# Optimization experiments

Hardware: AMD Instinct MI355X
Metric: run time of the kernel (lower is better)

## Reference

```python
import jax, jax.numpy as jnp
import numpy as np
from jax import lax

B, C, W, H = 32, 64, 32, 32
HEADS, RED = 4, 16
D = C // HEADS


def setup_inputs() -> dict:
    key = jax.random.key(0)
    ks = jax.random.split(key, 16)
    s = 0.05
    return {
        "x": jax.random.normal(ks[0], (B, C, W, H), jnp.float32),
        "Wq": jax.random.normal(ks[1], (C, C), jnp.float32) * s,
        "bq": jnp.zeros((C,), jnp.float32),
        "Wk": jax.random.normal(ks[2], (C, C), jnp.float32) * s,
        "bk": jnp.zeros((C,), jnp.float32),
        "Wv": jax.random.normal(ks[3], (C, C), jnp.float32) * s,
        "bv": jnp.zeros((C,), jnp.float32),
        "rel_h": jax.random.normal(ks[4], (1, HEADS, D, 1, H), jnp.float32),
        "rel_w": jax.random.normal(ks[5], (1, HEADS, D, W, 1), jnp.float32),
        "ln_g": jnp.ones((C, W, H), jnp.float32),
        "ln_b": jnp.zeros((C, W, H), jnp.float32),
        "ca_w1": jax.random.normal(ks[6], (C // RED, C), jnp.float32) * s,
        "ca_b1": jnp.zeros((C // RED,), jnp.float32),
        "ca_w2": jax.random.normal(ks[7], (C, C // RED), jnp.float32) * s,
        "ca_b2": jnp.zeros((C,), jnp.float32),
        "sa_w": jax.random.normal(ks[8], (1, 2, 7, 7), jnp.float32) * s,
        "sa_b": jnp.zeros((1,), jnp.float32),
    }


def reference(x, Wq, bq, Wk, bk, Wv, bv, rel_h, rel_w, ln_g, ln_b,
              ca_w1, ca_b1, ca_w2, ca_b2, sa_w, sa_b):
    b, c, w, h = x.shape
    n = w * h
    d = c // HEADS

    def conv1x1(t, wt, bt):
        return jnp.einsum('bchw,oc->bohw', t, wt) + bt[None, :, None, None]

    # ---- MHSA branch ----
    q = conv1x1(x, Wq, bq).reshape(b, HEADS, d, n)
    k = conv1x1(x, Wk, bk).reshape(b, HEADS, d, n)
    v = conv1x1(x, Wv, bv).reshape(b, HEADS, d, n)
    cc = jnp.einsum('bhdi,bhdj->bhij', q, k)                  # content-content
    pos = (rel_h + rel_w).reshape(1, HEADS, d, n)              # [1,H,d,N]
    cp = jnp.einsum('zhdi,bhdj->bhij', pos, q)                 # content-position
    att = jax.nn.softmax(cc + cp, axis=-1)                     # [b,H,N,N]
    out = jnp.einsum('bhdj,bhij->bhdi', v, att).reshape(b, c, w, h)
    # LayerNorm over (C,W,H)
    mu = jnp.mean(out, axis=(1, 2, 3), keepdims=True)
    var = jnp.var(out, axis=(1, 2, 3), keepdims=True)
    ln = (out - mu) * lax.rsqrt(var + 1e-5) * ln_g[None] + ln_b[None]
    mhsa = ln + x

    # ---- CBAM branch ----
    avg = jnp.mean(x, axis=(2, 3))                             # [b,c]
    mx = jnp.max(x, axis=(2, 3))

    def mlp(f):
        hid = jax.nn.relu(jnp.einsum('bc,oc->bo', f, ca_w1) + ca_b1)
        return jnp.einsum('bc,oc->bo', hid, ca_w2) + ca_b2

    ch_att = jax.nn.sigmoid(mlp(avg) + mlp(mx))[:, :, None, None]
    xc = ch_att * x
    feat = jnp.stack([jnp.mean(xc, axis=1), jnp.max(xc, axis=1)], axis=1)  # [b,2,w,h]
    sp = lax.conv_general_dilated(feat, sa_w, (1, 1), 'SAME',
                                  dimension_numbers=('NCHW', 'OIHW', 'NCHW'))
    sp = sp + sa_b[None, :, None, None]
    cbam = jax.nn.sigmoid(sp) * xc

    return mhsa + cbam + x
```

## Files before the change

kernel.cpp:

```cpp
#include <hip/hip_runtime.h>
#include <hip/hip_bf16.h>

#define BB 32
#define CC 64
#define WW 32
#define HHT 32
#define NH 4
#define DHD 16
#define NN 1024
#define LOG2E 1.4426950408889634f

typedef __attribute__((ext_vector_type(8))) short bf16x8;
typedef __attribute__((ext_vector_type(4))) float f32x4;

__device__ __forceinline__ float wave_sum(float v) {
#pragma unroll
  for (int off = 32; off > 0; off >>= 1) v += __shfl_down(v, off, 64);
  return v;
}
__device__ __forceinline__ float wave_max(float v) {
#pragma unroll
  for (int off = 32; off > 0; off >>= 1) v = fmaxf(v, __shfl_down(v, off, 64));
  return v;
}
__device__ __forceinline__ unsigned packbf2(float lo, float hi) {
  union { __hip_bfloat162 h; unsigned u; } c;
  c.h = __float22bfloat162_rn(float2{lo, hi});
  return c.u;
}
__device__ __forceinline__ short bf16s(float f) {
  unsigned a = __float_as_uint(f);
  a += 0x7FFFu + ((a >> 16) & 1u);
  return (short)(a >> 16);
}

__global__ __launch_bounds__(256) void qkv_kernel(
    const float* __restrict__ x,
    const float* __restrict__ Wq, const float* __restrict__ bq,
    const float* __restrict__ Wk, const float* __restrict__ bk,
    const float* __restrict__ Wv, const float* __restrict__ bv,
    short* __restrict__ KQ, short* __restrict__ Vb, float* __restrict__ lnzero)
{
  __shared__ __align__(16) short Ws[192 * 72];
  const int tid = threadIdx.x;
  const int b = blockIdx.y, nt = blockIdx.x;

  if (tid < 192) {
    const int m = tid >> 4, dd = tid & 15;
    const int mat = m >> 2, h = m & 3;
    const float* src = (mat == 0 ? Wk : (mat == 1 ? Wq : Wv)) + (h * 16 + dd) * CC;
    const float scale = (mat == 0) ? LOG2E : 1.f;
    short* dst = Ws + tid * 72;
#pragma unroll
    for (int c8 = 0; c8 < 8; ++c8) {
      const float4 f0 = *reinterpret_cast<const float4*>(src + c8 * 8);
      const float4 f1 = *reinterpret_cast<const float4*>(src + c8 * 8 + 4);
      uint4 u;
      u.x = packbf2(f0.x*scale, f0.y*scale); u.y = packbf2(f0.z*scale, f0.w*scale);
      u.z = packbf2(f1.x*scale, f1.y*scale); u.w = packbf2(f1.z*scale, f1.w*scale);
      *reinterpret_cast<uint4*>(dst + c8 * 8) = u;
    }
  }
  if (blockIdx.x == 0 && blockIdx.y == 0 && tid < 64) lnzero[tid] = 0.f;
  __syncthreads();

  const int wid = tid >> 6, lane = tid & 63, Q = lane >> 4, il = lane & 15;
  const int n = nt * 64 + wid * 16 + il;
  const float* xb = x + (size_t)b * CC * NN;

  union { bf16x8 s; unsigned u[4]; } bfr[2];
#pragma unroll
  for (int half = 0; half < 2; ++half) {
#pragma unroll
    for (int p = 0; p < 4; ++p) {
      const int c0 = 32 * half + 8 * Q + 2 * p;
      const float f0 = xb[(size_t)c0 * NN + n];
      const float f1 = xb[(size_t)(c0 + 1) * NN + n];
      bfr[half].u[p] = packbf2(f0, f1);
    }
  }

  const f32x4 zero4 = {0.f, 0.f, 0.f, 0.f};
  f32x4 acc[12];
#pragma unroll
  for (int m = 0; m < 12; ++m) {
    const short* wr = Ws + (m * 16 + il) * 72;
    const bf16x8 a0 = *reinterpret_cast<const bf16x8*>(wr + 8 * Q);
    const bf16x8 a1 = *reinterpret_cast<const bf16x8*>(wr + 32 + 8 * Q);
    acc[m] = __builtin_amdgcn_mfma_f32_16x16x32_bf16(a0, bfr[0].s, zero4, 0, 0, 0);
    acc[m] = __builtin_amdgcn_mfma_f32_16x16x32_bf16(a1, bfr[1].s, acc[m], 0, 0, 0);
  }

#pragma unroll
  for (int m = 0; m < 12; ++m) {
    const int mat = m >> 2, h = m & 3;
    const float bsc = (mat == 0) ? LOG2E : 1.f;
    const float4 bias = *reinterpret_cast<const float4*>(
        (mat == 0 ? bk : (mat == 1 ? bq : bv)) + h * 16 + 4 * Q);
    const float v0 = acc[m][0] + bias.x*bsc, v1 = acc[m][1] + bias.y*bsc;
    const float v2 = acc[m][2] + bias.z*bsc, v3 = acc[m][3] + bias.w*bsc;
    if (mat < 2) {
      uint2 pk;
      pk.x = packbf2(v0, v1); pk.y = packbf2(v2, v3);
      *reinterpret_cast<uint2*>(KQ + ((size_t)(b * NH + h) * NN + n) * 32 +
                                (mat == 0 ? 0 : 16) + 4 * Q) = pk;
    } else {
      short* vb = Vb + ((size_t)(b * NH + h) * 16 + 4 * Q) * NN + n;
      vb[0]            = bf16s(v0);
      vb[(size_t)NN]   = bf16s(v1);
      vb[2*(size_t)NN] = bf16s(v2);
      vb[3*(size_t)NN] = bf16s(v3);
    }
  }
}

__global__ __launch_bounds__(256, 3) void flash_kernel(
    const short* __restrict__ KQ, const short* __restrict__ Vb,
    const float* __restrict__ rel_h, const float* __restrict__ rel_w,
    float* __restrict__ attnout, float* __restrict__ lnsum, float* __restrict__ lnsum2)
{
  const int tid = threadIdx.x;
  const int wid = tid >> 6, lane = tid & 63;
  const int Q = lane >> 4, il = lane & 15;
  const int bh = blockIdx.x;
  const int h = bh & 3, b = bh >> 2;
  const int pr = wid & 1;
  const int jh = wid >> 1;
  const int ibase = blockIdx.y * 128 + pr * 64;
  const int j0base = jh * 512;

  bf16x8 bfrag[4];
#pragma unroll
  for (int g2 = 0; g2 < 4; ++g2) {
    const int i = ibase + g2*16 + il;
    if (Q < 2) {
      bfrag[g2] = *reinterpret_cast<const bf16x8*>(KQ + ((size_t)bh*NN + i)*32 + 16 + 8*Q);
    } else {
      const int wrow = i >> 5, hcol = i & 31;
      union { bf16x8 s; unsigned u[4]; } t;
#pragma unroll
      for (int p = 0; p < 4; ++p) {
        const int d0 = 8*(Q-2) + 2*p;
        const float f0 = LOG2E*(rel_h[(h*DHD + d0)*HHT + hcol] + rel_w[(h*DHD + d0)*WW + wrow]);
        const float f1 = LOG2E*(rel_h[(h*DHD + d0+1)*HHT + hcol] + rel_w[(h*DHD + d0+1)*WW + wrow]);
        t.u[p] = packbf2(f0, f1);
      }
      bfrag[g2] = t.s;
    }
  }

  const short* KQb = KQ + (size_t)bh*NN*32;
  const short* Vbb = Vb + ((size_t)bh*16 + il)*NN;
  const f32x4 zero4 = {0.f, 0.f, 0.f, 0.f};
  f32x4 acc[4]  = {zero4, zero4, zero4, zero4};
  f32x4 lacc[4] = {zero4, zero4, zero4, zero4};
  union u32x4 { bf16x8 s; unsigned u[4]; };
  u32x4 ones;
  ones.u[0] = ones.u[1] = ones.u[2] = ones.u[3] = 0x3F803F80u;

  bf16x8 agc[4], agn[4];
  u32x4 bv0c, bv1c, bv0n, bv1n;

#define LOADTILE(T, AG, BV0, BV1)                                              \
  {                                                                            \
    const int j0_ = j0base + ((T) & 7) * 64;                                   \
    _Pragma("unroll")                                                          \
    for (int g_ = 0; g_ < 4; ++g_)                                             \
      AG[g_] = *reinterpret_cast<const bf16x8*>(                               \
          KQb + (size_t)(j0_ + 16*g_ + il)*32 + 8*Q);                          \
    const short* vp_ = Vbb + j0_ + 4*Q;                                        \
    const uint2 l0_ = *reinterpret_cast<const uint2*>(vp_);                    \
    const uint2 h0_ = *reinterpret_cast<const uint2*>(vp_ + 16);               \
    const uint2 l1_ = *reinterpret_cast<const uint2*>(vp_ + 32);               \
    const uint2 h1_ = *reinterpret_cast<const uint2*>(vp_ + 48);               \
    BV0.u[0] = l0_.x; BV0.u[1] = l0_.y; BV0.u[2] = h0_.x; BV0.u[3] = h0_.y;    \
    BV1.u[0] = l1_.x; BV1.u[1] = l1_.y; BV1.u[2] = h1_.x; BV1.u[3] = h1_.y;    \
  }

#define FINISH(GP, B0, B1)                                                     \
  {                                                                            \
    unsigned pk_[4][2];                                                        \
    _Pragma("unroll")                                                          \
    for (int g_ = 0; g_ < 4; ++g_) {                                           \
      const float p0_ = __builtin_amdgcn_exp2f(sp[g_][0]);                     \
      const float p1_ = __builtin_amdgcn_exp2f(sp[g_][1]);                     \
      const float p2_ = __builtin_amdgcn_exp2f(sp[g_][2]);                     \
      const float p3_ = __builtin_amdgcn_exp2f(sp[g_][3]);                     \
      pk_[g_][0] = packbf2(p0_, p1_);                                          \
      pk_[g_][1] = packbf2(p2_, p3_);                                          \
    }                                                                          \
    u32x4 ap0_, ap1_;                                                          \
    ap0_.u[0] = pk_[0][0]; ap0_.u[1] = pk_[0][1];                              \
    ap0_.u[2] = pk_[1][0]; ap0_.u[3] = pk_[1][1];                              \
    ap1_.u[0] = pk_[2][0]; ap1_.u[1] = pk_[2][1];                              \
    ap1_.u[2] = pk_[3][0]; ap1_.u[3] = pk_[3][1];                              \
    acc[GP]  = __builtin_amdgcn_mfma_f32_16x16x32_bf16(ap0_.s, B0.s,  acc[GP], 0, 0, 0);  \
    lacc[GP] = __builtin_amdgcn_mfma_f32_16x16x32_bf16(ap0_.s, ones.s, lacc[GP], 0, 0, 0);\
    acc[GP]  = __builtin_amdgcn_mfma_f32_16x16x32_bf16(ap1_.s, B1.s,  acc[GP], 0, 0, 0);  \
    lacc[GP] = __builtin_amdgcn_mfma_f32_16x16x32_bf16(ap1_.s, ones.s, lacc[GP], 0, 0, 0);\
  }

  LOADTILE(0, agc, bv0c, bv1c);
  LOADTILE(1, agn, bv0n, bv1n);
  f32x4 sp[4];
#pragma unroll
  for (int g = 0; g < 4; ++g)
    sp[g] = __builtin_amdgcn_mfma_f32_16x16x32_bf16(agc[g], bfrag[0], zero4, 0, 0, 0);

  for (int t = 0; t < 8; ++t) {
#pragma unroll
    for (int g2 = 1; g2 < 4; ++g2) {
      f32x4 sn[4];
#pragma unroll
      for (int g = 0; g < 4; ++g)
        sn[g] = __builtin_amdgcn_mfma_f32_16x16x32_bf16(agc[g], bfrag[g2], zero4, 0, 0, 0);
      FINISH(g2 - 1, bv0c, bv1c);
#pragma unroll
      for (int g = 0; g < 4; ++g) sp[g] = sn[g];
    }
    if (t < 7) {
      u32x4 b0o = bv0c, b1o = bv1c;
#pragma unroll
      for (int g = 0; g < 4; ++g) agc[g] = agn[g];
      bv0c = bv0n; bv1c = bv1n;
      f32x4 sn[4];
#pragma unroll
      for (int g = 0; g < 4; ++g)
        sn[g] = __builtin_amdgcn_mfma_f32_16x16x32_bf16(agc[g], bfrag[0], zero4, 0, 0, 0);
      FINISH(3, b0o, b1o);
#pragma unroll
      for (int g = 0; g < 4; ++g) sp[g] = sn[g];
      LOADTILE(t + 2, agn, bv0n, bv1n);
    } else {
      FINISH(3, bv0c, bv1c);
    }
  }
#undef LOADTILE
#undef FINISH

  __shared__ float cmb[2][32][64];
  __shared__ float r1[2], r2[2];
  if (jh == 1) {
#pragma unroll
    for (int g2 = 0; g2 < 4; ++g2)
#pragma unroll
      for (int r = 0; r < 4; ++r) {
        cmb[pr][g2*4 + r][lane]      = acc[g2][r];
        cmb[pr][16 + g2*4 + r][lane] = lacc[g2][r];
      }
  }
  __syncthreads();
  if (jh == 0) {
    float s1 = 0.f, s2 = 0.f;
#pragma unroll
    for (int g2 = 0; g2 < 4; ++g2) {
      float4 vv;
      float* vp = &vv.x;
#pragma unroll
      for (int r = 0; r < 4; ++r) {
        const float num = acc[g2][r]  + cmb[pr][g2*4 + r][lane];
        const float den = lacc[g2][r] + cmb[pr][16 + g2*4 + r][lane];
        const float v = num / den;
        vp[r] = v;
        s1 += v; s2 += v*v;
      }
      *reinterpret_cast<float4*>(
          &attnout[((size_t)b*CC + h*DHD + il)*NN + ibase + g2*16 + 4*Q]) = vv;
    }
    s1 = wave_sum(s1); s2 = wave_sum(s2);
    if (lane == 0) { r1[pr] = s1; r2[pr] = s2; }
  }
  __syncthreads();
  if (tid == 0) {
    atomicAdd(&lnsum[b],  r1[0] + r1[1]);
    atomicAdd(&lnsum2[b], r2[0] + r2[1]);
  }
}

__global__ __launch_bounds__(256) void cbamstats_kernel(
    const float* __restrict__ x, float* __restrict__ avg, float* __restrict__ mx)
{
  const int bc = blockIdx.x, tid = threadIdx.x;
  const float* p = x + (size_t)bc*NN;
  float s = 0.f, m = -3.0e38f;
  for (int u = tid; u < NN; u += 256) { const float v = p[u]; s += v; m = fmaxf(m, v); }
  s = wave_sum(s); m = wave_max(m);
  __shared__ float rs[4], rm[4];
  const int wid = tid >> 6, lane = tid & 63;
  if (lane == 0) { rs[wid] = s; rm[wid] = m; }
  __syncthreads();
  if (tid == 0) {
    avg[bc] = (rs[0]+rs[1]+rs[2]+rs[3]) * (1.f/NN);
    mx[bc]  = fmaxf(fmaxf(rm[0], rm[1]), fmaxf(rm[2], rm[3]));
  }
}

__global__ __launch_bounds__(256) void mlpfeat_kernel(
    const float* __restrict__ x, const float* __restrict__ avg, const float* __restrict__ mxv,
    const float* __restrict__ w1, const float* __restrict__ b1,
    const float* __restrict__ w2, const float* __restrict__ b2,
    float* __restrict__ chv, float* __restrict__ feat)
{
  const int b = blockIdx.y, qq = blockIdx.x, tid = threadIdx.x;
  __shared__ float sa[CC], sm[CC], sch[CC];
  __shared__ float ps[4][64], pm[4][64];
  if (tid < CC) { sa[tid] = avg[b*CC + tid]; sm[tid] = mxv[b*CC + tid]; }
  __syncthreads();
  if (tid < CC) {
    float s = 2.f * b2[tid];
#pragma unroll
    for (int o = 0; o < 4; ++o) {
      float ha = b1[o], hm = b1[o];
#pragma unroll
      for (int k = 0; k < CC; ++k) { ha += w1[o*CC + k]*sa[k]; hm += w1[o*CC + k]*sm[k]; }
      s += w2[tid*4 + o] * (fmaxf(ha, 0.f) + fmaxf(hm, 0.f));
    }
    const float c = 1.f/(1.f + __expf(-s));
    sch[tid] = c;
    if (qq == 0) chv[b*CC + tid] = c;
  }
  __syncthreads();
  const int nl = tid & 63, cg = tid >> 6;
  const int n = qq*64 + nl;
  float s = 0.f, m = -3.0e38f;
#pragma unroll
  for (int c = cg*16; c < cg*16 + 16; ++c) {
    const float v = sch[c] * x[((size_t)b*CC + c)*NN + n];
    s += v; m = fmaxf(m, v);
  }
  ps[cg][nl] = s; pm[cg][nl] = m;
  __syncthreads();
  if (cg == 0) {
    const float S = ps[0][nl]+ps[1][nl]+ps[2][nl]+ps[3][nl];
    const float M = fmaxf(fmaxf(pm[0][nl], pm[1][nl]), fmaxf(pm[2][nl], pm[3][nl]));
    feat[(size_t)b*2*NN + n]      = S * (1.f/CC);
    feat[(size_t)b*2*NN + NN + n] = M;
  }
}

__global__ __launch_bounds__(256) void final_kernel(
    const float* __restrict__ x, const float* __restrict__ attn,
    const float* __restrict__ ln_g, const float* __restrict__ ln_b,
    const float* __restrict__ feat, const float* __restrict__ ch,
    const float* __restrict__ lnsum, const float* __restrict__ lnsum2,
    const float* __restrict__ sa_w, const float* __restrict__ sa_b,
    float* __restrict__ out)
{
  const int b = blockIdx.y;
  const int c0 = blockIdx.z * 16;
  const int n = blockIdx.x*256 + threadIdx.x;
  const int w = n >> 5, hh = n & 31;
  __shared__ float sch[CC];
  __shared__ float swt[98];
  if (threadIdx.x < CC) sch[threadIdx.x] = ch[b*CC + threadIdx.x];
  if (threadIdx.x < 98) swt[threadIdx.x] = sa_w[threadIdx.x];
  __syncthreads();

  float s = sa_b[0];
#pragma unroll
  for (int ci = 0; ci < 2; ++ci)
#pragma unroll
    for (int kh = 0; kh < 7; ++kh) {
      const int wy = w + kh - 3;
      if (wy < 0 || wy >= WW) continue;
#pragma unroll
      for (int kw = 0; kw < 7; ++kw) {
        const int hx = hh + kw - 3;
        if (hx < 0 || hx >= HHT) continue;
        s += feat[((size_t)(b*2) + ci)*NN + wy*HHT + hx] * swt[ci*49 + kh*7 + kw];
      }
    }
  const float sg = 1.f/(1.f + __expf(-s));
  const float inv = 1.f/(CC*NN);
  const float m = lnsum[b]*inv;
  const float var = lnsum2[b]*inv - m*m;
  const float r = rsqrtf(var + 1e-5f);
#pragma unroll
  for (int c = c0; c < c0 + 16; ++c) {
    const size_t idx = ((size_t)b*CC + c)*NN + n;
    const float xa = x[idx];
    const float ln = (attn[idx] - m) * r * ln_g[c*NN + n] + ln_b[c*NN + n];
    out[idx] = ln + 2.f*xa + sg * sch[c] * xa;
  }
}

extern "C" void kernel_launch(void* const* d_in, const int* in_sizes, int n_in,
                              void* d_out, int out_size, void* d_ws, size_t ws_size,
                              hipStream_t stream)
{
  const float* x     = (const float*)d_in[0];
  const float* Wq    = (const float*)d_in[1];
  const float* bq    = (const float*)d_in[2];
  const float* Wk    = (const float*)d_in[3];
  const float* bk    = (const float*)d_in[4];
  const float* Wv    = (const float*)d_in[5];
  const float* bv    = (const float*)d_in[6];
  const float* rel_h = (const float*)d_in[7];
  const float* rel_w = (const float*)d_in[8];
  const float* ln_g  = (const float*)d_in[9];
  const float* ln_b  = (const float*)d_in[10];
  const float* cw1   = (const float*)d_in[11];
  const float* cb1   = (const float*)d_in[12];
  const float* cw2   = (const float*)d_in[13];
  const float* cb2   = (const float*)d_in[14];
  const float* saw   = (const float*)d_in[15];
  const float* sab   = (const float*)d_in[16];
  float* out = (float*)d_out;

  short* KQ = (short*)d_ws;
  short* Vb = KQ + (size_t)128*1024*32;
  float* fs = (float*)(Vb + (size_t)128*16*1024);
  float* lnsum  = fs;
  float* lnsum2 = fs + 32;
  float* avg    = fs + 64;
  float* mxv    = avg + 2048;
  float* chv    = mxv + 2048;
  float* feat   = chv + 2048;
  float* attn   = out;

  qkv_kernel<<<dim3(16, BB), 256, 0, stream>>>(x, Wq, bq, Wk, bk, Wv, bv, KQ, Vb, lnsum);
  flash_kernel<<<dim3(BB*NH, 8), 256, 0, stream>>>(KQ, Vb, rel_h, rel_w, attn, lnsum, lnsum2);
  cbamstats_kernel<<<BB*CC, 256, 0, stream>>>(x, avg, mxv);
  mlpfeat_kernel<<<dim3(16, BB), 256, 0, stream>>>(x, avg, mxv, cw1, cb1, cw2, cb2, chv, feat);
  final_kernel<<<dim3(4, BB, 4), 256, 0, stream>>>(x, attn, ln_g, ln_b, feat, chv, lnsum, lnsum2, saw, sab, out);
}
```

Baseline: 165.0 us.

## Fuse CBAM channel avg/max stats into QKV kernel; raise flash occupancy

Removes the separate cbamstats kernel and computes per-channel sums and maxima inside the QKV projection kernel while x is already being loaded. It uses shared-memory atomics, with an order-preserving uint key for the max, then one global atomic per channel per block, and adds a memset to clear the accumulators. It also raises the flash kernel's launch-bounds min-blocks from 3 to 4 and skips an out-of-range tile prefetch on the second-to-last iteration. Risks are heavy LDS atomic contention, with every thread issuing 32 atomics, possible register spills from the higher occupancy target, and an extra memset launch.

```diff
diff --git a/kernel.cpp b/kernel.cpp
--- a/kernel.cpp
+++ b/kernel.cpp
@@ -18,11 +18,6 @@
   for (int off = 32; off > 0; off >>= 1) v += __shfl_down(v, off, 64);
   return v;
 }
-__device__ __forceinline__ float wave_max(float v) {
-#pragma unroll
-  for (int off = 32; off > 0; off >>= 1) v = fmaxf(v, __shfl_down(v, off, 64));
-  return v;
-}
 __device__ __forceinline__ unsigned packbf2(float lo, float hi) {
   union { __hip_bfloat162 h; unsigned u; } c;
   c.h = __float22bfloat162_rn(float2{lo, hi});
@@ -32,6 +27,13 @@
   unsigned a = __float_as_uint(f);
   a += 0x7FFFu + ((a >> 16) & 1u);
   return (short)(a >> 16);
+}
+__device__ __forceinline__ unsigned fkey(float f) {
+  const unsigned u = __float_as_uint(f);
+  return u ^ ((unsigned)((int)u >> 31) | 0x80000000u);
+}
+__device__ __forceinline__ float fkeyinv(unsigned k) {
+  return __uint_as_float((k & 0x80000000u) ? (k ^ 0x80000000u) : ~k);
 }
 
 __global__ __launch_bounds__(256) void qkv_kernel(
@@ -39,12 +41,16 @@
     const float* __restrict__ Wq, const float* __restrict__ bq,
     const float* __restrict__ Wk, const float* __restrict__ bk,
     const float* __restrict__ Wv, const float* __restrict__ bv,
-    short* __restrict__ KQ, short* __restrict__ Vb, float* __restrict__ lnzero)
+    short* __restrict__ KQ, short* __restrict__ Vb, float* __restrict__ lnzero,
+    float* __restrict__ avgs, unsigned* __restrict__ mxk)
 {
   __shared__ __align__(16) short Ws[192 * 72];
+  __shared__ float s_sum[CC];
+  __shared__ unsigned s_max[CC];
   const int tid = threadIdx.x;
   const int b = blockIdx.y, nt = blockIdx.x;
 
+  if (tid < CC) { s_sum[tid] = 0.f; s_max[tid] = 0u; }
   if (tid < 192) {
     const int m = tid >> 4, dd = tid & 15;
     const int mat = m >> 2, h = m & 3;
@@ -77,6 +83,10 @@
       const float f0 = xb[(size_t)c0 * NN + n];
       const float f1 = xb[(size_t)(c0 + 1) * NN + n];
       bfr[half].u[p] = packbf2(f0, f1);
+      atomicAdd(&s_sum[c0], f0);
+      atomicAdd(&s_sum[c0 + 1], f1);
+      atomicMax(&s_max[c0], fkey(f0));
+      atomicMax(&s_max[c0 + 1], fkey(f1));
     }
   }
 
@@ -112,9 +122,15 @@
       vb[3*(size_t)NN] = bf16s(v3);
     }
   }
-}
-
-__global__ __launch_bounds__(256, 3) void flash_kernel(
+
+  __syncthreads();
+  if (tid < CC) {
+    atomicAdd(&avgs[b * CC + tid], s_sum[tid]);
+    atomicMax(&mxk[b * CC + tid], s_max[tid]);
+  }
+}
+
+__global__ __launch_bounds__(256, 4) void flash_kernel(
     const short* __restrict__ KQ, const short* __restrict__ Vb,
     const float* __restrict__ rel_h, const float* __restrict__ rel_w,
     float* __restrict__ attnout, float* __restrict__ lnsum, float* __restrict__ lnsum2)
@@ -230,7 +246,7 @@
       FINISH(3, b0o, b1o);
 #pragma unroll
       for (int g = 0; g < 4; ++g) sp[g] = sn[g];
-      LOADTILE(t + 2, agn, bv0n, bv1n);
+      if (t < 6) LOADTILE(t + 2, agn, bv0n, bv1n);
     } else {
       FINISH(3, bv0c, bv1c);
     }
@@ -277,26 +293,8 @@
   }
 }
 
-__global__ __launch_bounds__(256) void cbamstats_kernel(
-    const float* __restrict__ x, float* __restrict__ avg, float* __restrict__ mx)
-{
-  const int bc = blockIdx.x, tid = threadIdx.x;
-  const float* p = x + (size_t)bc*NN;
-  float s = 0.f, m = -3.0e38f;
-  for (int u = tid; u < NN; u += 256) { const float v = p[u]; s += v; m = fmaxf(m, v); }
-  s = wave_sum(s); m = wave_max(m);
-  __shared__ float rs[4], rm[4];
-  const int wid = tid >> 6, lane = tid & 63;
-  if (lane == 0) { rs[wid] = s; rm[wid] = m; }
-  __syncthreads();
-  if (tid == 0) {
-    avg[bc] = (rs[0]+rs[1]+rs[2]+rs[3]) * (1.f/NN);
-    mx[bc]  = fmaxf(fmaxf(rm[0], rm[1]), fmaxf(rm[2], rm[3]));
-  }
-}
-
 __global__ __launch_bounds__(256) void mlpfeat_kernel(
-    const float* __restrict__ x, const float* __restrict__ avg, const float* __restrict__ mxv,
+    const float* __restrict__ x, const float* __restrict__ avgs, const unsigned* __restrict__ mxk,
     const float* __restrict__ w1, const float* __restrict__ b1,
     const float* __restrict__ w2, const float* __restrict__ b2,
     float* __restrict__ chv, float* __restrict__ feat)
@@ -304,7 +302,10 @@
   const int b = blockIdx.y, qq = blockIdx.x, tid = threadIdx.x;
   __shared__ float sa[CC], sm[CC], sch[CC];
   __shared__ float ps[4][64], pm[4][64];
-  if (tid < CC) { sa[tid] = avg[b*CC + tid]; sm[tid] = mxv[b*CC + tid]; }
+  if (tid < CC) {
+    sa[tid] = avgs[b*CC + tid] * (1.f/NN);
+    sm[tid] = fkeyinv(mxk[b*CC + tid]);
+  }
   __syncthreads();
   if (tid < CC) {
     float s = 2.f * b2[tid];
@@ -412,15 +413,16 @@
   float* fs = (float*)(Vb + (size_t)128*16*1024);
   float* lnsum  = fs;
   float* lnsum2 = fs + 32;
-  float* avg    = fs + 64;
-  float* mxv    = avg + 2048;
-  float* chv    = mxv + 2048;
+  float* avgs   = fs + 64;
+  unsigned* mxk = (unsigned*)(avgs + 2048);
+  float* chv    = avgs + 4096;
   float* feat   = chv + 2048;
   float* attn   = out;
 
-  qkv_kernel<<<dim3(16, BB), 256, 0, stream>>>(x, Wq, bq, Wk, bk, Wv, bv, KQ, Vb, lnsum);
+  hipMemsetAsync(avgs, 0, 4096 * sizeof(float), stream);
+
+  qkv_kernel<<<dim3(16, BB), 256, 0, stream>>>(x, Wq, bq, Wk, bk, Wv, bv, KQ, Vb, lnsum, avgs, mxk);
   flash_kernel<<<dim3(BB*NH, 8), 256, 0, stream>>>(KQ, Vb, rel_h, rel_w, attn, lnsum, lnsum2);
-  cbamstats_kernel<<<BB*CC, 256, 0, stream>>>(x, avg, mxv);
-  mlpfeat_kernel<<<dim3(16, BB), 256, 0, stream>>>(x, avg, mxv, cw1, cb1, cw2, cb2, chv, feat);
+  mlpfeat_kernel<<<dim3(16, BB), 256, 0, stream>>>(x, avgs, mxk, cw1, cb1, cw2, cb2, chv, feat);
   final_kernel<<<dim3(4, BB, 4), 256, 0, stream>>>(x, attn, ln_g, ln_b, feat, chv, lnsum, lnsum2, saw, sab, out);
 }
```

Result: slower. 204.4 us (+23.8%).
